# Kernel tuning notes

Hardware: AMD Instinct MI355X
Metric: run time of the kernel (lower is better)

Reference implementation:

```python
import jax, jax.numpy as jnp
import numpy as np

D, H, DK = 512, 8, 64
SCALE = 1.5 / 1.0  # gamma/tau, schedule='const'
NEG = -1e30


def _cross(x_q, x_kv, mask_kv, Wq, Wk, Wv, scale):
    # x_q: [B,Tq,D], x_kv: [B,Tk,D], mask_kv: [B,Tk] (1=keep, 0=mask)
    B, Tq, _ = x_q.shape
    Tk = x_kv.shape[1]
    q = (x_q @ Wq.T).reshape(B, Tq, H, DK).transpose(0, 2, 1, 3)
    k = (x_kv @ Wk.T).reshape(B, Tk, H, DK).transpose(0, 2, 1, 3)
    v = (x_kv @ Wv.T).reshape(B, Tk, H, DK).transpose(0, 2, 1, 3)
    logits = jnp.einsum('bhqd,bhkd->bhqk', q, k) * (scale / jnp.sqrt(jnp.float32(DK)))
    if mask_kv is not None:
        logits = jnp.where(mask_kv[:, None, None, :] == 0, NEG, logits)
    attn = jax.nn.softmax(logits, axis=-1)
    out = jnp.einsum('bhqk,bhkd->bhqd', attn, v)
    return out.transpose(0, 2, 1, 3).reshape(B, Tq, D)


def setup_inputs() -> dict:
    key = jax.random.key(0)
    ks = jax.random.split(key, 12)
    B, T = 4, 2048
    inp = {
        'skel_seq': jax.random.normal(ks[0], (B, T, D), jnp.float32),
        'sens_seq': jax.random.normal(ks[1], (B, T, D), jnp.float32),
        'mask_skel': jax.random.randint(ks[2], (B, T), 0, 2, jnp.int32),
        'mask_sens': jax.random.randint(ks[3], (B, T), 0, 2, jnp.int32),
    }
    s = 1.0 / np.sqrt(D)
    names = ['Wq_s2e', 'Wk_e', 'Wv_e', 'Wq_e2s', 'Wk_s', 'Wv_s', 'Wo_s', 'Wo_e']
    for i, n in enumerate(names):
        inp[n] = jax.random.normal(ks[4 + i], (D, D), jnp.float32) * s
    return inp


def reference(skel_seq, sens_seq, mask_skel, mask_sens,
              Wq_s2e, Wk_e, Wv_e, Wq_e2s, Wk_s, Wv_s, Wo_s, Wo_e):
    # skel queries attend over sensor keys/values
    s2e = _cross(skel_seq, sens_seq, mask_sens, Wq_s2e, Wk_e, Wv_e, SCALE) @ Wo_e.T
    # sensor queries attend over skeleton keys/values
    e2s = _cross(sens_seq, skel_seq, mask_skel, Wq_e2s, Wk_s, Wv_s, SCALE) @ Wo_s.T
    return (e2s, s2e)
```

## Files before the change

### kernel.cpp

```cpp
#include <hip/hip_runtime.h>
#include <hip/hip_bf16.h>

#define T_SEQ 2048
#define N_TOK 4194304
#define W_ELEM 262144


typedef float f32x4  __attribute__((ext_vector_type(4)));
typedef short bf16x8 __attribute__((ext_vector_type(8)));

#define SCALE_Q 0.27050532f

__device__ __forceinline__ unsigned short f2b(float f) {
    __hip_bfloat16 h = __float2bfloat16(f);
    return *reinterpret_cast<unsigned short*>(&h);
}

__device__ __forceinline__ int pack2bf(float lo, float hi) {
    return ((int)f2b(hi) << 16) | (int)f2b(lo);
}

__device__ __forceinline__ bf16x8 ldg8(const unsigned short* p) {
    union { int4 i; bf16x8 b; } u;
    u.i = *reinterpret_cast<const int4*>(p);
    return u.b;
}

__device__ __forceinline__ float fexp2(float x) {
#if __has_builtin(__builtin_amdgcn_exp2f)
    return __builtin_amdgcn_exp2f(x);
#else
    return exp2f(x);
#endif
}

typedef unsigned int u32_g __attribute__((address_space(1)));
typedef unsigned int u32_l __attribute__((address_space(3)));
__device__ __forceinline__ void gload_lds16(const void* g, void* l) {
    __builtin_amdgcn_global_load_lds((const u32_g*)g, (u32_l*)l, 16, 0, 0);
}

__global__ __launch_bounds__(256)
void prep_bias(const int* __restrict__ ms, const int* __restrict__ mk,
               float* __restrict__ dst)
{
    const int i = (blockIdx.x * 256 + threadIdx.x) * 8;
    const int* m = (i >> 13) ? mk : ms;
    const int rem = i & 8191;
    const int4 a = *reinterpret_cast<const int4*>(&m[rem]);
    const int4 b = *reinterpret_cast<const int4*>(&m[rem + 4]);
    float4 f0, f1;
    f0.x = a.x ? 0.0f : -3e38f; f0.y = a.y ? 0.0f : -3e38f;
    f0.z = a.z ? 0.0f : -3e38f; f0.w = a.w ? 0.0f : -3e38f;
    f1.x = b.x ? 0.0f : -3e38f; f1.y = b.y ? 0.0f : -3e38f;
    f1.z = b.z ? 0.0f : -3e38f; f1.w = b.w ? 0.0f : -3e38f;
    *reinterpret_cast<float4*>(&dst[i])     = f0;
    *reinterpret_cast<float4*>(&dst[i + 4]) = f1;
}

__global__ __launch_bounds__(256)
void to_bf16(const float* __restrict__ s0, const float* __restrict__ s1,
             const float* __restrict__ w0, const float* __restrict__ w1,
             const float* __restrict__ w2, const float* __restrict__ w3,
             const float* __restrict__ w4, const float* __restrict__ w5,
             unsigned short* __restrict__ dst)
{
    const int bid = blockIdx.x;
    int y, x;
    if (bid < 4096) { y = bid >> 11; x = bid & 2047; }
    else { const int t = bid - 4096; y = 2 + (t >> 7); x = t & 127; }
    const float* src;
    size_t off;
    switch (y) {
        case 0: src = s0; off = 0;      break;
        case 1: src = s1; off = N_TOK;  break;
        case 2: src = w0; off = 2 * (size_t)N_TOK;              break;
        case 3: src = w1; off = 2 * (size_t)N_TOK + 1 * W_ELEM; break;
        case 4: src = w2; off = 2 * (size_t)N_TOK + 2 * W_ELEM; break;
        case 5: src = w3; off = 2 * (size_t)N_TOK + 3 * W_ELEM; break;
        case 6: src = w4; off = 2 * (size_t)N_TOK + 4 * W_ELEM; break;
        default: src = w5; off = 2 * (size_t)N_TOK + 5 * W_ELEM; break;
    }
    const int idx = (x * 256 + threadIdx.x) * 8;
    const float4 a = *reinterpret_cast<const float4*>(src + idx);
    const float4 b = *reinterpret_cast<const float4*>(src + idx + 4);
    int4 o;
    o.x = pack2bf(a.x, a.y); o.y = pack2bf(a.z, a.w);
    o.z = pack2bf(b.x, b.y); o.w = pack2bf(b.z, b.w);
    *reinterpret_cast<int4*>(dst + off + idx) = o;
}

#define MF_SETUP                                                               \
    __shared__ short Asm[64][72];                                              \
    __shared__ short Wsm[64][72];                                              \
    const int tid  = threadIdx.x;                                              \
    const int lane = tid & 63;                                                 \
    const int w4   = tid >> 6;                                                 \
    const int nl   = lane & 15;                                                \
    const int quad = lane >> 4;                                                \
    const int n0 = blockIdx.x * 64;                                            \
    const int m0 = blockIdx.y * 64;                                            \
    const int arow = tid >> 2;                                                 \
    const int acol = (tid & 3) * 16;                                           \
    f32x4 acc[4] = {};

#define MF_WRITE_W                                                             \
    {                                                                          \
        int4 x;                                                                \
        x.x = pack2bf(wv[0].x, wv[0].y); x.y = pack2bf(wv[0].z, wv[0].w);      \
        x.z = pack2bf(wv[1].x, wv[1].y); x.w = pack2bf(wv[1].z, wv[1].w);      \
        *reinterpret_cast<int4*>(&Wsm[arow][acol]) = x;                        \
        x.x = pack2bf(wv[2].x, wv[2].y); x.y = pack2bf(wv[2].z, wv[2].w);      \
        x.z = pack2bf(wv[3].x, wv[3].y); x.w = pack2bf(wv[3].z, wv[3].w);      \
        *reinterpret_cast<int4*>(&Wsm[arow][acol + 8]) = x;                    \
    }

#define MF_MMA_LOOP                                                            \
    _Pragma("unroll")                                                          \
    for (int kc = 0; kc < 2; ++kc) {                                           \
        const bf16x8 a = *reinterpret_cast<const bf16x8*>(                     \
            &Asm[w4 * 16 + nl][kc * 32 + quad * 8]);                           \
        _Pragma("unroll")                                                      \
        for (int c = 0; c < 4; ++c) {                                          \
            const bf16x8 bf = *reinterpret_cast<const bf16x8*>(                \
                &Wsm[c * 16 + nl][kc * 32 + quad * 8]);                        \
            acc[c] = __builtin_amdgcn_mfma_f32_16x16x32_bf16(a, bf, acc[c],    \
                                                             0, 0, 0);         \
        }                                                                      \
    }

#define MF_CWRITE_PROJ                                                         \
    if (!trans) {                                                              \
        _Pragma("unroll")                                                      \
        for (int c = 0; c < 4; ++c)                                            \
            _Pragma("unroll")                                                  \
            for (int r = 0; r < 4; ++r)                                        \
                C[(size_t)(m0 + w4 * 16 + quad * 4 + r) * 512 + n0 + c * 16 + nl] = \
                    f2b(acc[c][r] * alpha);                                    \
    } else {                                                                   \
        const int b  = m0 >> 11;                                               \
        const int t0 = (m0 & 2047) + w4 * 16 + quad * 4;                       \
        _Pragma("unroll")                                                      \
        for (int c = 0; c < 4; ++c) {                                          \
            const int n = n0 + c * 16 + nl;                                    \
            ushort4 o;                                                         \
            o.x = f2b(acc[c][0]);                                              \
            o.y = f2b(acc[c][1]);                                              \
            o.z = f2b(acc[c][2]);                                              \
            o.w = f2b(acc[c][3]);                                              \
            *reinterpret_cast<ushort4*>(C + (size_t)(b * 512 + n) * T_SEQ + t0) = o; \
        }                                                                      \
    }

__global__ __launch_bounds__(256)
void proj_all(const float* __restrict__ skel, const float* __restrict__ sens,
              const float* __restrict__ Wq1, const float* __restrict__ Wk1,
              const float* __restrict__ Wv1, const float* __restrict__ Wq2,
              const float* __restrict__ Wk2, const float* __restrict__ Wv2,
              unsigned short* __restrict__ Q1, unsigned short* __restrict__ K1,
              unsigned short* __restrict__ Vt1, unsigned short* __restrict__ Q2,
              unsigned short* __restrict__ K2, unsigned short* __restrict__ Vt2,
              int zbase)
{
    const int z = zbase + blockIdx.z;
    const float* A; const float* W; unsigned short* C;
    float alpha = 1.0f; bool trans = false;
    switch (z) {
        case 0:  A = skel; W = Wq1; C = Q1; alpha = SCALE_Q; break;
        case 1:  A = sens; W = Wk1; C = K1; break;
        case 2:  A = sens; W = Wv1; C = Vt1; trans = true; break;
        case 3:  A = sens; W = Wq2; C = Q2; alpha = SCALE_Q; break;
        case 4:  A = skel; W = Wk2; C = K2; break;
        default: A = skel; W = Wv2; C = Vt2; trans = true; break;
    }

    MF_SETUP
    const float* ap = A + (size_t)(m0 + arow) * 512 + acol;
    const float* wp = W + (size_t)(n0 + arow) * 512 + acol;
    float4 av[4], wv[4];
    #pragma unroll
    for (int j = 0; j < 4; ++j) {
        av[j] = *reinterpret_cast<const float4*>(ap + 4 * j);
        wv[j] = *reinterpret_cast<const float4*>(wp + 4 * j);
    }
    for (int it = 0; it < 8; ++it) {
        __syncthreads();
        {
            int4 x;
            x.x = pack2bf(av[0].x, av[0].y); x.y = pack2bf(av[0].z, av[0].w);
            x.z = pack2bf(av[1].x, av[1].y); x.w = pack2bf(av[1].z, av[1].w);
            *reinterpret_cast<int4*>(&Asm[arow][acol]) = x;
            x.x = pack2bf(av[2].x, av[2].y); x.y = pack2bf(av[2].z, av[2].w);
            x.z = pack2bf(av[3].x, av[3].y); x.w = pack2bf(av[3].z, av[3].w);
            *reinterpret_cast<int4*>(&Asm[arow][acol + 8]) = x;
        }
        MF_WRITE_W
        __syncthreads();
        if (it < 7) {
            const float* apn = ap + (it + 1) * 64;
            const float* wpn = wp + (it + 1) * 64;
            #pragma unroll
            for (int j = 0; j < 4; ++j) {
                av[j] = *reinterpret_cast<const float4*>(apn + 4 * j);
                wv[j] = *reinterpret_cast<const float4*>(wpn + 4 * j);
            }
        }
        MF_MMA_LOOP
    }
    MF_CWRITE_PROJ
}

__global__ __launch_bounds__(256, 2)
void proj_fused(const unsigned short* __restrict__ skb,
                const unsigned short* __restrict__ snb,
                const unsigned short* __restrict__ wball,
                unsigned short* __restrict__ Q1, unsigned short* __restrict__ K1,
                unsigned short* __restrict__ Vt1, unsigned short* __restrict__ Q2,
                unsigned short* __restrict__ K2, unsigned short* __restrict__ Vt2)
{
    __shared__ __align__(16) char smem[65536];
    short (*Al)[128][64] = reinterpret_cast<short (*)[128][64]>(smem);
    short (*Wl)[128][64] = reinterpret_cast<short (*)[128][64]>(smem + 32768);

    const int o   = blockIdx.x;
    const int wg  = (o & 7) * 192 + (o >> 3);
    const int z   = wg >> 8;
    const int idx = wg & 255;
    const int nh  = idx & 3;
    const int mt  = idx >> 2;

    const unsigned short* A = (z == 0 || z >= 4) ? skb : snb;
    const unsigned short* W = wball + (size_t)z * W_ELEM;
    unsigned short* C;
    switch (z) {
        case 0: C = Q1;  break;
        case 1: C = K1;  break;
        case 2: C = Vt1; break;
        case 3: C = Q2;  break;
        case 4: C = K2;  break;
        default: C = Vt2; break;
    }
    const bool trans = (z == 2 || z == 5);
    const float alpha = (z == 0 || z == 3) ? SCALE_Q : 1.0f;

    const int tid  = threadIdx.x;
    const int w    = tid >> 6;
    const int wr   = w >> 1;
    const int wc   = w & 1;
    const int lane = tid & 63;
    const int nl   = lane & 15;
    const int quad = lane >> 4;
    const int r8   = lane >> 3;
    const int cg   = (lane & 7) ^ r8;

    const int m0g = mt * 128;
    const int n0  = nh * 128;

    const unsigned short* Ab = A + (size_t)m0g * 512 + cg * 8;
    const unsigned short* Wb = W + (size_t)n0  * 512 + cg * 8;

    f32x4 acc[4][4] = {};

    auto stage = [&](int it, int buf) {
        const int k0 = it * 64;
        #pragma unroll
        for (int g = 0; g < 4; ++g) {
            const int rr = w * 32 + g * 8;
            gload_lds16(Ab + (size_t)(rr + r8) * 512 + k0, &Al[buf][rr][0]);
            gload_lds16(Wb + (size_t)(rr + r8) * 512 + k0, &Wl[buf][rr][0]);
        }
    };

    stage(0, 0);
    asm volatile("s_waitcnt vmcnt(0)" ::: "memory");
    __syncthreads();

    const int sw = nl & 7;
    for (int it = 0; it < 8; ++it) {
        const int buf = it & 1;
        if (it < 7) stage(it + 1, buf ^ 1);
        #pragma unroll
        for (int kc = 0; kc < 2; ++kc) {
            bf16x8 a[4], bb[4];
            #pragma unroll
            for (int am = 0; am < 4; ++am)
                a[am] = *reinterpret_cast<const bf16x8*>(
                    &Al[buf][wr * 64 + am * 16 + nl][((kc * 4 + quad) ^ sw) * 8]);
            #pragma unroll
            for (int bn = 0; bn < 4; ++bn)
                bb[bn] = *reinterpret_cast<const bf16x8*>(
                    &Wl[buf][wc * 64 + bn * 16 + nl][((kc * 4 + quad) ^ sw) * 8]);
            #pragma unroll
            for (int am = 0; am < 4; ++am)
                #pragma unroll
                for (int bn = 0; bn < 4; ++bn)
                    acc[am][bn] = __builtin_amdgcn_mfma_f32_16x16x32_bf16(
                        a[am], bb[bn], acc[am][bn], 0, 0, 0);
        }
        asm volatile("s_waitcnt vmcnt(0)" ::: "memory");
        __syncthreads();
    }

    if (!trans) {
        short (*Cl)[132] = reinterpret_cast<short (*)[132]>(smem);
        #pragma unroll
        for (int am = 0; am < 4; ++am)
            #pragma unroll
            for (int bn = 0; bn < 4; ++bn)
                #pragma unroll
                for (int r = 0; r < 4; ++r)
                    Cl[wr * 64 + am * 16 + quad * 4 + r][wc * 64 + bn * 16 + nl] =
                        (short)f2b(acc[am][bn][r] * alpha);
        __syncthreads();
        const int lr = tid >> 1;
        const int ch = (tid & 1) * 64;
        unsigned short* cp = C + (size_t)(m0g + lr) * 512 + n0 + ch;
        #pragma unroll
        for (int j = 0; j < 8; ++j)
            *reinterpret_cast<int4*>(cp + j * 8) =
                *reinterpret_cast<const int4*>(&Cl[lr][ch + j * 8]);
    } else {
        short (*Tl)[132] = reinterpret_cast<short (*)[132]>(smem);
        #pragma unroll
        for (int am = 0; am < 4; ++am)
            #pragma unroll
            for (int bn = 0; bn < 4; ++bn) {
                int* dst = reinterpret_cast<int*>(
                    &Tl[wc * 64 + bn * 16 + nl][wr * 64 + am * 16 + quad * 4]);
                dst[0] = pack2bf(acc[am][bn][0], acc[am][bn][1]);
                dst[1] = pack2bf(acc[am][bn][2], acc[am][bn][3]);
            }
        __syncthreads();
        const int bq = m0g >> 11;
        const int t0 = m0g & 2047;
        const int nr = tid >> 1;
        const int tc = (tid & 1) * 64;
        unsigned short* vp = C + (size_t)(bq * 512 + n0 + nr) * T_SEQ + t0 + tc;
        #pragma unroll
        for (int j = 0; j < 8; ++j)
            *reinterpret_cast<int4*>(vp + j * 8) =
                *reinterpret_cast<const int4*>(&Tl[nr][tc + j * 8]);
    }
}

__global__ __launch_bounds__(256, 2)
void out_fused(const unsigned short* __restrict__ AO1, const float* __restrict__ Wo1,
               float* __restrict__ C1,
               const unsigned short* __restrict__ AO2, const float* __restrict__ Wo2,
               float* __restrict__ C2)
{
    __shared__ __align__(16) char smem[67584];
    short (*Al)[128][64] = reinterpret_cast<short (*)[128][64]>(smem);
    short (*Wl)[128][64] = reinterpret_cast<short (*)[128][64]>(smem + 32768);

    const int o   = blockIdx.x;
    const int wg  = (o & 7) * 64 + (o >> 3);
    const int z   = wg >> 8;
    const int idx = wg & 255;
    const int nh  = idx & 3;
    const int mt  = idx >> 2;

    const unsigned short* A = z ? AO2 : AO1;
    const float* W = z ? Wo2 : Wo1;
    float* C = z ? C2 : C1;

    const int tid  = threadIdx.x;
    const int w    = tid >> 6;
    const int wr   = w >> 1;
    const int wc   = w & 1;
    const int lane = tid & 63;
    const int nl   = lane & 15;
    const int quad = lane >> 4;
    const int r8   = lane >> 3;
    const int cg   = (lane & 7) ^ r8;

    const int m0g = mt * 128;
    const int n0  = nh * 128;

    const unsigned short* Ab = A + (size_t)m0g * 512 + cg * 8;

    const int rw_ = tid >> 1;
    const int ch_ = (tid & 1) * 32;
    const int key = rw_ & 7;

    f32x4 acc[4][4] = {};
    float4 wreg[8];

    auto stageA = [&](int it, int buf) {
        const int k0 = it * 64;
        #pragma unroll
        for (int g = 0; g < 4; ++g) {
            const int rr = w * 32 + g * 8;
            gload_lds16(Ab + (size_t)(rr + r8) * 512 + k0, &Al[buf][rr][0]);
        }
    };
    auto wload = [&](int it) {
        const float* wp = W + (size_t)(n0 + rw_) * 512 + it * 64 + ch_;
        #pragma unroll
        for (int j = 0; j < 8; ++j)
            wreg[j] = *reinterpret_cast<const float4*>(wp + 4 * j);
    };
    auto wstore = [&](int buf) {
        #pragma unroll
        for (int j = 0; j < 8; ++j) {
            int2 pk;
            pk.x = pack2bf(wreg[j].x, wreg[j].y);
            pk.y = pack2bf(wreg[j].z, wreg[j].w);
            const int slot = ((tid & 1) * 4 + (j >> 1)) ^ key;
            *reinterpret_cast<int2*>(
                &Wl[buf][rw_][slot * 8 + (j & 1) * 4]) = pk;
        }
    };

    wload(0);
    stageA(0, 0);
    asm volatile("s_waitcnt vmcnt(0)" ::: "memory");
    wstore(0);
    __syncthreads();

    const int sw = nl & 7;
    for (int it = 0; it < 8; ++it) {
        const int buf = it & 1;
        if (it < 7) { stageA(it + 1, buf ^ 1); wload(it + 1); }
        #pragma unroll
        for (int kc = 0; kc < 2; ++kc) {
            bf16x8 a[4], bb[4];
            #pragma unroll
            for (int am = 0; am < 4; ++am)
                a[am] = *reinterpret_cast<const bf16x8*>(
                    &Al[buf][wr * 64 + am * 16 + nl][((kc * 4 + quad) ^ sw) * 8]);
            #pragma unroll
            for (int bn = 0; bn < 4; ++bn)
                bb[bn] = *reinterpret_cast<const bf16x8*>(
                    &Wl[buf][wc * 64 + bn * 16 + nl][((kc * 4 + quad) ^ sw) * 8]);
            #pragma unroll
            for (int am = 0; am < 4; ++am)
                #pragma unroll
                for (int bn = 0; bn < 4; ++bn)
                    acc[am][bn] = __builtin_amdgcn_mfma_f32_16x16x32_bf16(
                        a[am], bb[bn], acc[am][bn], 0, 0, 0);
        }
        asm volatile("s_waitcnt vmcnt(0)" ::: "memory");
        if (it < 7) wstore(buf ^ 1);
        __syncthreads();
    }

    float (*Cl)[132] = reinterpret_cast<float (*)[132]>(smem);
    #pragma unroll
    for (int am = 0; am < 4; ++am)
        #pragma unroll
        for (int bn = 0; bn < 4; ++bn)
            #pragma unroll
            for (int r = 0; r < 4; ++r)
                Cl[wr * 64 + am * 16 + quad * 4 + r][wc * 64 + bn * 16 + nl] =
                    acc[am][bn][r];
    __syncthreads();
    const int lr = tid >> 1;
    const int fc = (tid & 1) * 64;
    float* cp = C + (size_t)(m0g + lr) * 512 + n0 + fc;
    #pragma unroll
    for (int j = 0; j < 16; ++j)
        *reinterpret_cast<float4*>(cp + j * 4) =
            *reinterpret_cast<const float4*>(&Cl[lr][fc + j * 4]);
}

__global__ __launch_bounds__(256)
void out_proj(const unsigned short* __restrict__ AO1, const float* __restrict__ Wo1,
              float* __restrict__ C1,
              const unsigned short* __restrict__ AO2, const float* __restrict__ Wo2,
              float* __restrict__ C2, int zbase)
{
    const int z = zbase + blockIdx.z;
    const unsigned short* A = z ? AO2 : AO1;
    const float* W = z ? Wo2 : Wo1;
    float* C = z ? C2 : C1;

    MF_SETUP
    const unsigned short* ap = A + (size_t)(m0 + arow) * 512 + acol;
    const float* wp = W + (size_t)(n0 + arow) * 512 + acol;
    int4 ai[2];
    float4 wv[4];
    ai[0] = *reinterpret_cast<const int4*>(ap);
    ai[1] = *reinterpret_cast<const int4*>(ap + 8);
    #pragma unroll
    for (int j = 0; j < 4; ++j)
        wv[j] = *reinterpret_cast<const float4*>(wp + 4 * j);
    for (int it = 0; it < 8; ++it) {
        __syncthreads();
        *reinterpret_cast<int4*>(&Asm[arow][acol])     = ai[0];
        *reinterpret_cast<int4*>(&Asm[arow][acol + 8]) = ai[1];
        MF_WRITE_W
        __syncthreads();
        if (it < 7) {
            const unsigned short* apn = ap + (it + 1) * 64;
            const float* wpn = wp + (it + 1) * 64;
            ai[0] = *reinterpret_cast<const int4*>(apn);
            ai[1] = *reinterpret_cast<const int4*>(apn + 8);
            #pragma unroll
            for (int j = 0; j < 4; ++j)
                wv[j] = *reinterpret_cast<const float4*>(wpn + 4 * j);
        }
        MF_MMA_LOOP
    }
    #pragma unroll
    for (int c = 0; c < 4; ++c)
        #pragma unroll
        for (int r = 0; r < 4; ++r)
            C[(size_t)(m0 + w4 * 16 + quad * 4 + r) * 512 + n0 + c * 16 + nl] =
                acc[c][r];
}

__global__ __launch_bounds__(512)
void attn_mfma(const unsigned short* Q1x, const unsigned short* __restrict__ K1x,
               const unsigned short* __restrict__ V1x, const float* __restrict__ b1x,
               unsigned short* AO1x,
               const unsigned short* Q2x, const unsigned short* __restrict__ K2x,
               const unsigned short* __restrict__ V2x, const float* __restrict__ b2x,
               unsigned short* AO2x)
{
    __shared__ short Kl[2][64][64];
    __shared__ short Vl[2][64][64];
    __shared__ short Pl[8][16][64];

    const int dir = blockIdx.y >> 5;
    const unsigned short* Q  = dir ? Q2x : Q1x;
    const unsigned short* K  = dir ? K2x : K1x;
    const unsigned short* Vt = dir ? V2x : V1x;
    const float* biasD       = dir ? b2x : b1x;
    unsigned short* AO       = dir ? AO2x : AO1x;

    const int tid  = threadIdx.x;
    const int w    = tid >> 6;
    const int lane = tid & 63;
    const int nl   = lane & 15;
    const int quad = lane >> 4;
    const int qt = blockIdx.x;
    const int bh = blockIdx.y & 31;
    const int b = bh >> 3, h = bh & 7;
    const size_t tb = (size_t)b * (T_SEQ * 512);
    const float* biasB = biasD + b * T_SEQ;

    const int r8 = lane >> 3;
    const int cg = (lane & 7) ^ r8;
    const int sr = w * 8;

    const unsigned short* qp = Q + tb + (size_t)(qt * 128 + w * 16 + nl) * 512 + h * 64 + quad * 8;
    const bf16x8 qb0 = ldg8(qp);
    const bf16x8 qb1 = ldg8(qp + 32);

    float l_run = 0.0f;
    f32x4 o[4] = {};

    gload_lds16(K  + tb + (size_t)(sr + r8) * 512 + h * 64 + cg * 8, &Kl[0][sr][0]);
    gload_lds16(Vt + (size_t)(b * 512 + h * 64 + sr + r8) * T_SEQ + cg * 8, &Vl[0][sr][0]);
    asm volatile("s_waitcnt vmcnt(0)" ::: "memory");
    __syncthreads();

    const int swz = nl & 7;

    for (int kt = 0; kt < 32; ++kt) {
        const int cur = kt & 1;
        short (*Kb)[64] = Kl[cur];
        short (*Vb)[64] = Vl[cur];

        if (kt < 31) {
            short (*Kn)[64] = Kl[cur ^ 1];
            short (*Vn)[64] = Vl[cur ^ 1];
            gload_lds16(K  + tb + (size_t)((kt + 1) * 64 + sr + r8) * 512 + h * 64 + cg * 8, &Kn[sr][0]);
            gload_lds16(Vt + (size_t)(b * 512 + h * 64 + sr + r8) * T_SEQ + (size_t)(kt + 1) * 64 + cg * 8, &Vn[sr][0]);
        }

        float p[4][4];
        #pragma unroll
        for (int s = 0; s < 4; ++s) {
            const bf16x8 k0 = *reinterpret_cast<const bf16x8*>(&Kb[s * 16 + nl][(quad ^ swz) * 8]);
            const bf16x8 k1 = *reinterpret_cast<const bf16x8*>(&Kb[s * 16 + nl][((4 + quad) ^ swz) * 8]);
            const float4 bb = *reinterpret_cast<const float4*>(
                &biasB[kt * 64 + s * 16 + quad * 4]);
            f32x4 z = {bb.x, bb.y, bb.z, bb.w};
            z = __builtin_amdgcn_mfma_f32_16x16x32_bf16(k0, qb0, z, 0, 0, 0);
            z = __builtin_amdgcn_mfma_f32_16x16x32_bf16(k1, qb1, z, 0, 0, 0);
            p[s][0] = fexp2(z[0]);
            p[s][1] = fexp2(z[1]);
            p[s][2] = fexp2(z[2]);
            p[s][3] = fexp2(z[3]);
            l_run += p[s][0] + p[s][1] + p[s][2] + p[s][3];
        }

        #pragma unroll
        for (int s = 0; s < 4; ++s) {
            int2 pk;
            pk.x = pack2bf(p[s][0], p[s][1]);
            pk.y = pack2bf(p[s][2], p[s][3]);
            const int slot = (2 * s + (quad >> 1)) ^ swz;
            *reinterpret_cast<int2*>(&Pl[w][nl][slot * 8 + (quad & 1) * 4]) = pk;
        }

        const bf16x8 pa0 = *reinterpret_cast<const bf16x8*>(&Pl[w][nl][(quad ^ swz) * 8]);
        const bf16x8 pa1 = *reinterpret_cast<const bf16x8*>(&Pl[w][nl][((4 + quad) ^ swz) * 8]);
        __builtin_amdgcn_s_setprio(1);
        #pragma unroll
        for (int sd = 0; sd < 4; ++sd) {
            const bf16x8 v0 = *reinterpret_cast<const bf16x8*>(&Vb[sd * 16 + nl][(quad ^ swz) * 8]);
            const bf16x8 v1 = *reinterpret_cast<const bf16x8*>(&Vb[sd * 16 + nl][((4 + quad) ^ swz) * 8]);
            o[sd] = __builtin_amdgcn_mfma_f32_16x16x32_bf16(v0, pa0, o[sd], 0, 0, 0);
            o[sd] = __builtin_amdgcn_mfma_f32_16x16x32_bf16(v1, pa1, o[sd], 0, 0, 0);
        }
        __builtin_amdgcn_s_setprio(0);

        asm volatile("s_waitcnt vmcnt(0)" ::: "memory");
        __syncthreads();
    }

    l_run += __shfl_xor(l_run, 16);
    l_run += __shfl_xor(l_run, 32);
    const float inv = 1.0f / l_run;
    unsigned short* ob = AO + tb + (size_t)(qt * 128 + w * 16 + nl) * 512 + h * 64 + quad * 4;
    #pragma unroll
    for (int sd = 0; sd < 4; ++sd) {
        ushort4 o4;
        o4.x = f2b(o[sd][0] * inv);
        o4.y = f2b(o[sd][1] * inv);
        o4.z = f2b(o[sd][2] * inv);
        o4.w = f2b(o[sd][3] * inv);
        *reinterpret_cast<ushort4*>(ob + sd * 16) = o4;
    }
}

extern "C" void kernel_launch(void* const* d_in, const int* in_sizes, int n_in,
                              void* d_out, int out_size, void* d_ws, size_t ws_size,
                              hipStream_t stream) {
    const float* skel = (const float*)d_in[0];
    const float* sens = (const float*)d_in[1];
    const int* mask_skel = (const int*)d_in[2];
    const int* mask_sens = (const int*)d_in[3];
    const float* Wq_s2e = (const float*)d_in[4];
    const float* Wk_e   = (const float*)d_in[5];
    const float* Wv_e   = (const float*)d_in[6];
    const float* Wq_e2s = (const float*)d_in[7];
    const float* Wk_s   = (const float*)d_in[8];
    const float* Wv_s   = (const float*)d_in[9];
    const float* Wo_s   = (const float*)d_in[10];
    const float* Wo_e   = (const float*)d_in[11];
    float* out = (float*)d_out;

    unsigned short* Q1 = (unsigned short*)d_ws;
    unsigned short* K1 = Q1 + N_TOK;
    unsigned short* V1 = K1 + N_TOK;

    const bool big = ws_size >= (size_t)6 * N_TOK * sizeof(unsigned short);

    if (big) {
        unsigned short* Q2 = V1 + N_TOK;
        unsigned short* K2 = Q2 + N_TOK;
        unsigned short* V2 = K2 + N_TOK;
        unsigned short* SC  = (unsigned short*)d_out;
        unsigned short* skb = SC;
        unsigned short* snb = SC + N_TOK;
        unsigned short* wb  = SC + 2 * (size_t)N_TOK;
        float* biasS = (float*)(SC + 2 * (size_t)N_TOK + 6 * W_ELEM);
        float* bias0 = biasS;
        float* bias1 = biasS + 4 * T_SEQ;
        prep_bias<<<dim3(8), 256, 0, stream>>>(mask_sens, mask_skel, biasS);
        to_bf16<<<dim3(4864), 256, 0, stream>>>(
            skel, sens, Wq_s2e, Wk_e, Wv_e, Wq_e2s, Wk_s, Wv_s, SC);
        proj_fused<<<dim3(1536), 256, 0, stream>>>(
            skb, snb, wb, Q1, K1, V1, Q2, K2, V2);
        attn_mfma<<<dim3(16, 64), 512, 0, stream>>>(
            Q1, K1, V1, bias0, Q1,
            Q2, K2, V2, bias1, Q2);
        out_fused<<<dim3(512), 256, 0, stream>>>(
            Q1, Wo_e, out + N_TOK, Q2, Wo_s, out);
    } else {
        float* bias0 = out;
        float* bias1 = out + 8192;
        prep_bias<<<dim3(8), 256, 0, stream>>>(mask_sens, mask_skel, bias0);
        proj_all<<<dim3(8, 128, 3), 256, 0, stream>>>(
            skel, sens, Wq_s2e, Wk_e, Wv_e, Wq_e2s, Wk_s, Wv_s,
            Q1, K1, V1, Q1, K1, V1, 0);
        attn_mfma<<<dim3(16, 32), 512, 0, stream>>>(
            Q1, K1, V1, bias0, Q1, Q1, K1, V1, bias0, Q1);
        out_proj<<<dim3(8, 128, 1), 256, 0, stream>>>(
            Q1, Wo_e, out + N_TOK, Q1, Wo_s, out, 0);
        proj_all<<<dim3(8, 128, 3), 256, 0, stream>>>(
            skel, sens, Wq_s2e, Wk_e, Wv_e, Wq_e2s, Wk_s, Wv_s,
            Q1, K1, V1, Q1, K1, V1, 3);
        attn_mfma<<<dim3(16, 32), 512, 0, stream>>>(
            Q1, K1, V1, bias1, Q1, Q1, K1, V1, bias1, Q1);
        out_proj<<<dim3(8, 128, 1), 256, 0, stream>>>(
            Q1, Wo_s, out, Q1, Wo_s, out, 1);
    }
}
```

Before: 300.9 us.

## Triple-buffer projection GEMM with smaller K tiles and raw barriers

Restructures the fused QKV projection GEMM main loop from double-buffered 64-wide K tiles into triple-buffered 32-wide K tiles with prefetch two stages ahead. It waits with partial vmcnt and uses a bare s_barrier in place of __syncthreads. Shared memory drops to 48KB so launch bounds can request 3 blocks per CU. The LDS swizzle and the epilogue row padding are changed to match. The aim is to hide global-to-LDS latency and raise occupancy, at the cost of more barriers per K and fewer MFMAs between syncs.

```diff
diff --git a/kernel.cpp b/kernel.cpp
--- a/kernel.cpp
+++ b/kernel.cpp
@@ -38,6 +38,12 @@
 typedef unsigned int u32_l __attribute__((address_space(3)));
 __device__ __forceinline__ void gload_lds16(const void* g, void* l) {
     __builtin_amdgcn_global_load_lds((const u32_g*)g, (u32_l*)l, 16, 0, 0);
+}
+
+__device__ __forceinline__ void raw_barrier() {
+    __builtin_amdgcn_sched_barrier(0);
+    __builtin_amdgcn_s_barrier();
+    __builtin_amdgcn_sched_barrier(0);
 }
 
 __global__ __launch_bounds__(256)
@@ -210,7 +216,7 @@
     MF_CWRITE_PROJ
 }
 
-__global__ __launch_bounds__(256, 2)
+__global__ __launch_bounds__(256, 3)
 void proj_fused(const unsigned short* __restrict__ skb,
                 const unsigned short* __restrict__ snb,
                 const unsigned short* __restrict__ wball,
@@ -218,9 +224,9 @@
                 unsigned short* __restrict__ Vt1, unsigned short* __restrict__ Q2,
                 unsigned short* __restrict__ K2, unsigned short* __restrict__ Vt2)
 {
-    __shared__ __align__(16) char smem[65536];
-    short (*Al)[128][64] = reinterpret_cast<short (*)[128][64]>(smem);
-    short (*Wl)[128][64] = reinterpret_cast<short (*)[128][64]>(smem + 32768);
+    __shared__ __align__(16) char smem[49152];
+    short (*Al)[128][32] = reinterpret_cast<short (*)[128][32]>(smem);
+    short (*Wl)[128][32] = reinterpret_cast<short (*)[128][32]>(smem + 24576);
 
     const int o   = blockIdx.x;
     const int wg  = (o & 7) * 192 + (o >> 3);
@@ -250,59 +256,60 @@
     const int lane = tid & 63;
     const int nl   = lane & 15;
     const int quad = lane >> 4;
-    const int r8   = lane >> 3;
-    const int cg   = (lane & 7) ^ r8;
+    const int rof  = lane >> 2;
+    const int cg   = (lane & 3) ^ ((lane >> 3) & 3);
 
     const int m0g = mt * 128;
     const int n0  = nh * 128;
 
-    const unsigned short* Ab = A + (size_t)m0g * 512 + cg * 8;
-    const unsigned short* Wb = W + (size_t)n0  * 512 + cg * 8;
+    const unsigned short* srcA0 = A + (size_t)(m0g + w * 32 + rof) * 512 + cg * 8;
+    const unsigned short* srcA1 = srcA0 + (size_t)16 * 512;
+    const unsigned short* srcW0 = W + (size_t)(n0 + w * 32 + rof) * 512 + cg * 8;
+    const unsigned short* srcW1 = srcW0 + (size_t)16 * 512;
 
     f32x4 acc[4][4] = {};
 
     auto stage = [&](int it, int buf) {
-        const int k0 = it * 64;
-        #pragma unroll
-        for (int g = 0; g < 4; ++g) {
-            const int rr = w * 32 + g * 8;
-            gload_lds16(Ab + (size_t)(rr + r8) * 512 + k0, &Al[buf][rr][0]);
-            gload_lds16(Wb + (size_t)(rr + r8) * 512 + k0, &Wl[buf][rr][0]);
-        }
+        const int k0 = it * 32;
+        gload_lds16(srcA0 + k0, &Al[buf][w * 32][0]);
+        gload_lds16(srcA1 + k0, &Al[buf][w * 32 + 16][0]);
+        gload_lds16(srcW0 + k0, &Wl[buf][w * 32][0]);
+        gload_lds16(srcW1 + k0, &Wl[buf][w * 32 + 16][0]);
     };
 
     stage(0, 0);
-    asm volatile("s_waitcnt vmcnt(0)" ::: "memory");
-    __syncthreads();
-
-    const int sw = nl & 7;
-    for (int it = 0; it < 8; ++it) {
-        const int buf = it & 1;
-        if (it < 7) stage(it + 1, buf ^ 1);
-        #pragma unroll
-        for (int kc = 0; kc < 2; ++kc) {
-            bf16x8 a[4], bb[4];
-            #pragma unroll
-            for (int am = 0; am < 4; ++am)
-                a[am] = *reinterpret_cast<const bf16x8*>(
-                    &Al[buf][wr * 64 + am * 16 + nl][((kc * 4 + quad) ^ sw) * 8]);
+    stage(1, 1);
+    asm volatile("s_waitcnt vmcnt(4)" ::: "memory");
+    raw_barrier();
+
+    const int key = (nl >> 1) & 3;
+    int bcur = 0, bpre = 2;
+    for (int it = 0; it < 16; ++it) {
+        if (it < 14) stage(it + 2, bpre);
+        bf16x8 a[4], bb[4];
+        #pragma unroll
+        for (int am = 0; am < 4; ++am)
+            a[am] = *reinterpret_cast<const bf16x8*>(
+                &Al[bcur][wr * 64 + am * 16 + nl][(quad ^ key) * 8]);
+        #pragma unroll
+        for (int bn = 0; bn < 4; ++bn)
+            bb[bn] = *reinterpret_cast<const bf16x8*>(
+                &Wl[bcur][wc * 64 + bn * 16 + nl][(quad ^ key) * 8]);
+        #pragma unroll
+        for (int am = 0; am < 4; ++am)
             #pragma unroll
             for (int bn = 0; bn < 4; ++bn)
-                bb[bn] = *reinterpret_cast<const bf16x8*>(
-                    &Wl[buf][wc * 64 + bn * 16 + nl][((kc * 4 + quad) ^ sw) * 8]);
-            #pragma unroll
-            for (int am = 0; am < 4; ++am)
-                #pragma unroll
-                for (int bn = 0; bn < 4; ++bn)
-                    acc[am][bn] = __builtin_amdgcn_mfma_f32_16x16x32_bf16(
-                        a[am], bb[bn], acc[am][bn], 0, 0, 0);
-        }
-        asm volatile("s_waitcnt vmcnt(0)" ::: "memory");
-        __syncthreads();
+                acc[am][bn] = __builtin_amdgcn_mfma_f32_16x16x32_bf16(
+                    a[am], bb[bn], acc[am][bn], 0, 0, 0);
+        if (it < 14)       asm volatile("s_waitcnt vmcnt(4)" ::: "memory");
+        else if (it == 14) asm volatile("s_waitcnt vmcnt(0)" ::: "memory");
+        raw_barrier();
+        bcur = (bcur == 2) ? 0 : bcur + 1;
+        bpre = (bpre == 2) ? 0 : bpre + 1;
     }
 
     if (!trans) {
-        short (*Cl)[132] = reinterpret_cast<short (*)[132]>(smem);
+        short (*Cl)[136] = reinterpret_cast<short (*)[136]>(smem);
         #pragma unroll
         for (int am = 0; am < 4; ++am)
             #pragma unroll
@@ -320,7 +327,7 @@
             *reinterpret_cast<int4*>(cp + j * 8) =
                 *reinterpret_cast<const int4*>(&Cl[lr][ch + j * 8]);
     } else {
-        short (*Tl)[132] = reinterpret_cast<short (*)[132]>(smem);
+        short (*Tl)[136] = reinterpret_cast<short (*)[136]>(smem);
         #pragma unroll
         for (int am = 0; am < 4; ++am)
             #pragma unroll
```

After: 283.9 us. 5.6% less time.
